# Kernel optimization log

Measured on AMD Instinct MI355X. Metric: run time of the kernel, lower is better.

Reference implementation:

```python
import jax, jax.numpy as jnp
import numpy as np

B, T, H, V = 64, 128, 50, 8192  # batch, window, lstm hidden (=embedding_size=50 in source), vocab
REC_DROP, DENSE_DROP = 0.3, 0.5


def setup_inputs() -> dict:
    key = jax.random.key(0)
    ks = jax.random.split(key, 16)
    n = lambda k, *s: 0.1 * jax.random.normal(k, s, dtype=jnp.float32)
    inp = {}
    inp["batched_input"] = jax.random.randint(ks[0], (B, T), 0, V)
    inp["E"] = n(ks[1], V, H)                  # embedding table
    inp["Wx"] = n(ks[2], H, 4 * H)             # LSTM input kernel (i,f,c,o)
    inp["U"] = n(ks[3], 4, H, H)               # LSTM recurrent kernel per gate
    inp["b"] = jnp.zeros((4 * H,), jnp.float32)
    inp["W1"] = n(ks[4], H, V)                 # denseTypeOne, first application
    inp["b1"] = jnp.zeros((V,), jnp.float32)   # shared bias (layer reused)
    inp["W1b"] = n(ks[5], V, V)                # denseTypeOne, second application (V->V)
    inp["W2"] = n(ks[6], V, V)                 # denseTypeTwo (sigmoid)
    inp["b2"] = jnp.zeros((V,), jnp.float32)
    # Frozen dropout masks (inverted-dropout scaling baked in).
    inp["rec_mask"] = jax.random.bernoulli(ks[7], 1.0 - REC_DROP, (4, B, H)).astype(jnp.float32) / (1.0 - REC_DROP)
    inp["dmask1"] = jax.random.bernoulli(ks[8], 1.0 - DENSE_DROP, (B, T // 2, V)).astype(jnp.float32) / (1.0 - DENSE_DROP)
    inp["dmask2"] = jax.random.bernoulli(ks[9], 1.0 - DENSE_DROP, (B, T // 2, V)).astype(jnp.float32) / (1.0 - DENSE_DROP)
    return inp


def _lstm(emb, Wx, U, b, rec_mask):
    # emb: [B,T,H]; precompute input contribution once, scan over time.
    zx = jnp.einsum('bth,hk->tbk', emb, Wx) + b  # [T,B,4H]

    def step(carry, z_t):
        h, c = carry
        # per-gate recurrent dropout on h, as Keras does off the cuDNN path
        rec = jnp.einsum('gbh,ghk->bgk', h[None, :, :] * rec_mask, U)  # [B,4,H]
        z = z_t.reshape(B, 4, H) + rec
        i = jax.nn.sigmoid(z[:, 0])
        f = jax.nn.sigmoid(z[:, 1])
        g = jnp.tanh(z[:, 2])
        o = jax.nn.sigmoid(z[:, 3])
        c_new = f * c + i * g
        h_new = o * jnp.tanh(c_new)
        return (h_new, c_new), h_new

    init = (jnp.zeros((B, H), emb.dtype), jnp.zeros((B, H), emb.dtype))
    _, hs = jax.lax.scan(step, init, zx)  # [T,B,H]
    return jnp.transpose(hs, (1, 0, 2))   # [B,T,H]


def reference(batched_input, E, Wx, U, b, W1, b1, W1b, W2, b2, rec_mask, dmask1, dmask2):
    emb = E[batched_input]                       # [B,T,H]
    seq = _lstm(emb, Wx, U, b, rec_mask)         # [B,T,H]
    pooled = seq.reshape(B, T // 2, 2, H).max(axis=2)  # MaxPool1D(pool=2)
    d1 = jax.nn.relu(pooled @ W1 + b1)           # [B,T/2,V]
    x = d1 * dmask1                              # dropout 0.5 (training=True)
    d2 = jax.nn.relu(x @ W1b + b1)               # denseTypeOne reused (shared bias)
    x = d2 * dmask2
    prbs = jax.nn.sigmoid(x @ W2 + b2)           # [B,T/2,V]
    return prbs
```

## Files before the change

### kernel.cpp

```cpp
#include <hip/hip_runtime.h>


#define Bc 64
#define Tc 128
#define Hc 50
#define Vc 8192
#define Mrows 4096

typedef unsigned short u16;
typedef short bf16x8 __attribute__((ext_vector_type(8)));
typedef float f32x4 __attribute__((ext_vector_type(4)));

__device__ __forceinline__ u16 f2bf(float x) {
  union { float f; unsigned int u; } v; v.f = x;
  unsigned int r = v.u + 0x7fffu + ((v.u >> 16) & 1u);
  return (u16)(r >> 16);
}

__device__ __forceinline__ void async_copy16(void* lds, const void* g) {
  __builtin_amdgcn_global_load_lds(
      (const __attribute__((address_space(1))) void*)g,
      (__attribute__((address_space(3))) void*)lds, 16, 0, 0);
}

__device__ __forceinline__ float sigmoidf(float x) {
  return 1.0f / (1.0f + __expf(-x));
}

__global__ __launch_bounds__(256) void zx_kernel(
    const int* __restrict__ tok, const float* __restrict__ E,
    const float* __restrict__ Wx, const float* __restrict__ bvec,
    float* __restrict__ zx) {
  const int tb = blockIdx.x;
  const int t = tb >> 6, b = tb & 63;
  __shared__ float e_s[Hc];
  const int id = tok[b * Tc + t];
  if (threadIdx.x < Hc) e_s[threadIdx.x] = E[id * Hc + threadIdx.x];
  __syncthreads();
  if (threadIdx.x < 4 * Hc) {
    float acc = bvec[threadIdx.x];
    #pragma unroll
    for (int h = 0; h < Hc; ++h) acc += e_s[h] * Wx[h * 200 + threadIdx.x];
    zx[(size_t)tb * 200 + threadIdx.x] = acc;
  }
}

__global__ __launch_bounds__(256) void lstm_kernel(
    const float* __restrict__ zx, const float* __restrict__ U,
    const float* __restrict__ rec_mask, u16* __restrict__ pooled) {
  const int b = blockIdx.x;
  const int tid = threadIdx.x;
  __shared__ float Us[4 * Hc * Hc];
  __shared__ float recm[4 * Hc];
  __shared__ float h_s[Hc], c_s[Hc], hprev[Hc];
  __shared__ float hm[4 * Hc], z_s[4 * Hc];

  for (int i = tid; i < 4 * Hc * Hc; i += 256) Us[i] = U[i];
  if (tid < 200) recm[tid] = rec_mask[(tid / Hc) * Bc * Hc + b * Hc + (tid % Hc)];
  if (tid < Hc) { h_s[tid] = 0.f; c_s[tid] = 0.f; }
  __syncthreads();

  for (int t = 0; t < Tc; ++t) {
    if (tid < 200) hm[tid] = h_s[tid % Hc] * recm[tid];
    __syncthreads();
    if (tid < 200) {
      const int g = tid / Hc, k = tid % Hc;
      float acc = zx[((size_t)t * Bc + b) * 200 + tid];
      const float* Ug = Us + g * Hc * Hc;
      const float* hmg = hm + g * Hc;
      #pragma unroll
      for (int h = 0; h < Hc; ++h) acc += hmg[h] * Ug[h * Hc + k];
      z_s[tid] = acc;
    }
    __syncthreads();
    if (tid < Hc) {
      const int k = tid;
      const float i_ = sigmoidf(z_s[k]);
      const float f_ = sigmoidf(z_s[Hc + k]);
      const float g_ = tanhf(z_s[2 * Hc + k]);
      const float o_ = sigmoidf(z_s[3 * Hc + k]);
      const float c = f_ * c_s[k] + i_ * g_;
      const float h = o_ * tanhf(c);
      c_s[k] = c; h_s[k] = h;
      if ((t & 1) != 0) {
        pooled[((size_t)b * 64 + (t >> 1)) * 64 + k] = f2bf(fmaxf(hprev[k], h));
      } else {
        hprev[k] = h;
      }
    }
    if ((t & 1) != 0 && tid >= Hc && tid < 64)
      pooled[((size_t)b * 64 + (t >> 1)) * 64 + tid] = 0;
    __syncthreads();
  }
}

__global__ __launch_bounds__(256) void w1t_kernel(
    const float* __restrict__ W1, u16* __restrict__ W1T) {
  const int idx = blockIdx.x * 256 + threadIdx.x;
  const int n = idx >> 6, k = idx & 63;
  const float v = (k < Hc) ? W1[(size_t)k * Vc + n] : 0.f;
  W1T[idx] = f2bf(v);
}

__global__ __launch_bounds__(256) void wt_kernel(
    const float* __restrict__ W, u16* __restrict__ WT) {
  __shared__ float sm[128][65];
  const int t = threadIdx.x;
  const size_t k0 = (size_t)blockIdx.x * 128;
  const size_t n0 = (size_t)blockIdx.y * 64;
  {
    const int n = t & 63, kr = t >> 6;
    #pragma unroll
    for (int i = 0; i < 32; ++i) {
      const int k = i * 4 + kr;
      sm[k][n] = W[(k0 + k) * Vc + n0 + n];
    }
  }
  __syncthreads();
  {
    const int kk = (t & 63) * 2, nr = t >> 6;
    #pragma unroll
    for (int i = 0; i < 16; ++i) {
      const int nn = i * 4 + nr;
      ushort2 v;
      v.x = f2bf(sm[kk][nn]);
      v.y = f2bf(sm[kk + 1][nn]);
      *(ushort2*)&WT[(n0 + nn) * Vc + k0 + kk] = v;
    }
  }
}

template <bool SIGMOID>
__global__ __launch_bounds__(256, 2) void gemm_bt(
    const u16* __restrict__ A, const u16* __restrict__ Bt,
    const float* __restrict__ bias, const float* __restrict__ mask,
    void* __restrict__ Cout, const int M, const int N, const int K) {
  __shared__ u16 As[128 * 64];
  __shared__ u16 Bs[128 * 64];
  const int tid = threadIdx.x;
  const int wave = tid >> 6;
  const int lane = tid & 63;
  const int wr = (wave >> 1) << 6;
  const int wc = (wave & 1) << 6;
  const long tileM = (long)blockIdx.y * 128;
  const long tileN = (long)blockIdx.x * 128;

  const int lrow = lane >> 3;
  const int cg8 = (((lane & 7) ^ lrow) << 3);
  const u16* Ab = A + tileM * K;
  const u16* Bb = Bt + tileN * K;

  f32x4 acc[4][4] = {};

  for (int k0 = 0; k0 < K; k0 += 64) {
    #pragma unroll
    for (int q4 = 0; q4 < 4; ++q4) {
      const int r = (wave << 5) + (q4 << 3) + lrow;
      const int ldsoff = (wave * 4 + q4) << 10;
      async_copy16((char*)As + ldsoff, Ab + (long)r * K + k0 + cg8);
      async_copy16((char*)Bs + ldsoff, Bb + (long)r * K + k0 + cg8);
    }
    __syncthreads();
    #pragma unroll
    for (int kk = 0; kk < 64; kk += 32) {
      const int ch = (kk >> 3) + (lane >> 4);
      bf16x8 af[4], bf[4];
      #pragma unroll
      for (int i = 0; i < 4; ++i) {
        const int ra = wr + (i << 4) + (lane & 15);
        af[i] = *(const bf16x8*)(As + ra * 64 + ((ch ^ (ra & 7)) << 3));
      }
      #pragma unroll
      for (int j = 0; j < 4; ++j) {
        const int rb = wc + (j << 4) + (lane & 15);
        bf[j] = *(const bf16x8*)(Bs + rb * 64 + ((ch ^ (rb & 7)) << 3));
      }
      #pragma unroll
      for (int i = 0; i < 4; ++i)
        #pragma unroll
        for (int j = 0; j < 4; ++j)
          acc[i][j] = __builtin_amdgcn_mfma_f32_16x16x32_bf16(af[i], bf[j], acc[i][j], 0, 0, 0);
    }
    __syncthreads();
  }

  const int qrow = (lane >> 4) << 2;
  const int qcol = lane & 15;
  #pragma unroll
  for (int j = 0; j < 4; ++j) {
    const long col = tileN + wc + (j << 4) + qcol;
    const float bv = bias[col];
    #pragma unroll
    for (int i = 0; i < 4; ++i) {
      const long row0 = tileM + wr + (i << 4) + qrow;
      #pragma unroll
      for (int r = 0; r < 4; ++r) {
        const long off = (row0 + r) * N + col;
        const float z = acc[i][j][r] + bv;
        if constexpr (SIGMOID) {
          ((float*)Cout)[off] = sigmoidf(z);
        } else {
          ((u16*)Cout)[off] = f2bf(fmaxf(z, 0.f) * mask[off]);
        }
      }
    }
  }
}

extern "C" void kernel_launch(void* const* d_in, const int* in_sizes, int n_in,
                              void* d_out, int out_size, void* d_ws, size_t ws_size,
                              hipStream_t stream) {
  const int*   tok  = (const int*)  d_in[0];
  const float* E    = (const float*)d_in[1];
  const float* Wx   = (const float*)d_in[2];
  const float* U    = (const float*)d_in[3];
  const float* bvec = (const float*)d_in[4];
  const float* W1   = (const float*)d_in[5];
  const float* b1   = (const float*)d_in[6];
  const float* W1b  = (const float*)d_in[7];
  const float* W2   = (const float*)d_in[8];
  const float* b2   = (const float*)d_in[9];
  const float* recm = (const float*)d_in[10];
  const float* dm1  = (const float*)d_in[11];
  const float* dm2  = (const float*)d_in[12];
  float* out = (float*)d_out;

  char* w = (char*)d_ws;
  u16* Wt     = (u16*)w;  w += (size_t)Vc * Vc * 2;
  u16* A1     = (u16*)w;  w += (size_t)Mrows * Vc * 2;
  u16* A2     = (u16*)w;  w += (size_t)Mrows * Vc * 2;
  u16* W1T    = (u16*)w;  w += (size_t)Vc * 64 * 2;
  u16* pooled = (u16*)w;  w += (size_t)Mrows * 64 * 2;
  float* zx   = (float*)w;

  zx_kernel  <<<Bc * Tc, 256, 0, stream>>>(tok, E, Wx, bvec, zx);
  lstm_kernel<<<Bc, 256, 0, stream>>>(zx, U, recm, pooled);
  w1t_kernel <<<(Vc * 64) / 256, 256, 0, stream>>>(W1, W1T);
  gemm_bt<false><<<dim3(Vc / 128, Mrows / 128), 256, 0, stream>>>(
      pooled, W1T, b1, dm1, A1, Mrows, Vc, 64);
  wt_kernel<<<dim3(Vc / 128, Vc / 64), 256, 0, stream>>>(W1b, Wt);
  gemm_bt<false><<<dim3(Vc / 128, Mrows / 128), 256, 0, stream>>>(
      A1, Wt, b1, dm2, A2, Mrows, Vc, Vc);
  wt_kernel<<<dim3(Vc / 128, Vc / 64), 256, 0, stream>>>(W2, Wt);
  gemm_bt<true><<<dim3(Vc / 128, Mrows / 128), 256, 0, stream>>>(
      A2, Wt, b2, nullptr, out, Mrows, Vc, Vc);
}
```

Before: 2.048 ms.

## Rewrite LSTM recurrence as single-wave kernel with register-resident weights and readlane broadcast

Measured after the change: 2.070 ms. Within noise of the previous version (+1.1%).

```diff
diff --git a/kernel.cpp b/kernel.cpp
--- a/kernel.cpp
+++ b/kernel.cpp
@@ -25,6 +25,16 @@
 
 __device__ __forceinline__ float sigmoidf(float x) {
   return 1.0f / (1.0f + __expf(-x));
+}
+
+__device__ __forceinline__ float tanh_fast(float x) {
+  x = fminf(fmaxf(x, -15.f), 15.f);
+  const float e = __expf(-2.f * x);
+  return (1.f - e) / (1.f + e);
+}
+
+__device__ __forceinline__ float readlane_f(float v, int l) {
+  return __uint_as_float(__builtin_amdgcn_readlane(__float_as_uint(v), l));
 }
 
 __global__ __launch_bounds__(256) void zx_kernel(
@@ -45,52 +55,62 @@
   }
 }
 
-__global__ __launch_bounds__(256) void lstm_kernel(
+__global__ __launch_bounds__(64) void lstm_kernel(
     const float* __restrict__ zx, const float* __restrict__ U,
     const float* __restrict__ rec_mask, u16* __restrict__ pooled) {
   const int b = blockIdx.x;
-  const int tid = threadIdx.x;
-  __shared__ float Us[4 * Hc * Hc];
-  __shared__ float recm[4 * Hc];
-  __shared__ float h_s[Hc], c_s[Hc], hprev[Hc];
-  __shared__ float hm[4 * Hc], z_s[4 * Hc];
-
-  for (int i = tid; i < 4 * Hc * Hc; i += 256) Us[i] = U[i];
-  if (tid < 200) recm[tid] = rec_mask[(tid / Hc) * Bc * Hc + b * Hc + (tid % Hc)];
-  if (tid < Hc) { h_s[tid] = 0.f; c_s[tid] = 0.f; }
+  const int lane = threadIdx.x;
+  __shared__ float zs[Tc * 200 + 64];
+
+  for (int i = lane; i < Tc * 50; i += 64) {
+    const int t = i / 50, j = i % 50;
+    ((float4*)zs)[t * 50 + j] = ((const float4*)zx)[((size_t)t * Bc + b) * 50 + j];
+  }
+
+  float rm[4];
+  #pragma unroll
+  for (int g = 0; g < 4; ++g)
+    rm[g] = (lane < Hc) ? rec_mask[((size_t)g * Bc + b) * Hc + lane] : 0.f;
+
+  float Um[4][Hc];
+  #pragma unroll
+  for (int g = 0; g < 4; ++g) {
+    #pragma unroll
+    for (int h = 0; h < Hc; ++h) {
+      const float u = (lane < Hc) ? U[((size_t)g * Hc + h) * Hc + lane] : 0.f;
+      Um[g][h] = u * readlane_f(rm[g], h);
+    }
+  }
   __syncthreads();
 
+  float hreg = 0.f, creg = 0.f, hprev = 0.f;
+  const int zlane = (lane < Hc) ? lane : Hc - 1;
   for (int t = 0; t < Tc; ++t) {
-    if (tid < 200) hm[tid] = h_s[tid % Hc] * recm[tid];
-    __syncthreads();
-    if (tid < 200) {
-      const int g = tid / Hc, k = tid % Hc;
-      float acc = zx[((size_t)t * Bc + b) * 200 + tid];
-      const float* Ug = Us + g * Hc * Hc;
-      const float* hmg = hm + g * Hc;
-      #pragma unroll
-      for (int h = 0; h < Hc; ++h) acc += hmg[h] * Ug[h * Hc + k];
-      z_s[tid] = acc;
-    }
-    __syncthreads();
-    if (tid < Hc) {
-      const int k = tid;
-      const float i_ = sigmoidf(z_s[k]);
-      const float f_ = sigmoidf(z_s[Hc + k]);
-      const float g_ = tanhf(z_s[2 * Hc + k]);
-      const float o_ = sigmoidf(z_s[3 * Hc + k]);
-      const float c = f_ * c_s[k] + i_ * g_;
-      const float h = o_ * tanhf(c);
-      c_s[k] = c; h_s[k] = h;
-      if ((t & 1) != 0) {
-        pooled[((size_t)b * 64 + (t >> 1)) * 64 + k] = f2bf(fmaxf(hprev[k], h));
-      } else {
-        hprev[k] = h;
-      }
-    }
-    if ((t & 1) != 0 && tid >= Hc && tid < 64)
-      pooled[((size_t)b * 64 + (t >> 1)) * 64 + tid] = 0;
-    __syncthreads();
+    const float z0 = zs[t * 200 + 0 * Hc + zlane];
+    const float z1 = zs[t * 200 + 1 * Hc + zlane];
+    const float z2 = zs[t * 200 + 2 * Hc + zlane];
+    const float z3 = zs[t * 200 + 3 * Hc + zlane];
+    float a0 = 0.f, a1 = 0.f, a2 = 0.f, a3 = 0.f;
+    #pragma unroll
+    for (int h = 0; h < Hc; ++h) {
+      const float hv = readlane_f(hreg, h);
+      a0 += hv * Um[0][h];
+      a1 += hv * Um[1][h];
+      a2 += hv * Um[2][h];
+      a3 += hv * Um[3][h];
+    }
+    const float i_ = sigmoidf(z0 + a0);
+    const float f_ = sigmoidf(z1 + a1);
+    const float g_ = tanh_fast(z2 + a2);
+    const float o_ = sigmoidf(z3 + a3);
+    creg = f_ * creg + i_ * g_;
+    hreg = o_ * tanh_fast(creg);
+    if (t & 1) {
+      const size_t po = ((size_t)b * 64 + (t >> 1)) * 64 + lane;
+      pooled[po] = (lane < Hc) ? f2bf(fmaxf(hprev, hreg)) : (u16)0;
+    } else {
+      hprev = hreg;
+    }
   }
 }
 
@@ -234,7 +254,7 @@
   float* zx   = (float*)w;
 
   zx_kernel  <<<Bc * Tc, 256, 0, stream>>>(tok, E, Wx, bvec, zx);
-  lstm_kernel<<<Bc, 256, 0, stream>>>(zx, U, recm, pooled);
+  lstm_kernel<<<Bc, 64, 0, stream>>>(zx, U, recm, pooled);
   w1t_kernel <<<(Vc * 64) / 256, 256, 0, stream>>>(W1, W1T);
   gemm_bt<false><<<dim3(Vc / 128, Mrows / 128), 256, 0, stream>>>(
       pooled, W1T, b1, dm1, A1, Mrows, Vc, 64);
```
